# Performance work log

Measured on AMD Instinct MI355X. Metric: run time of the kernel, lower is better.

The kernel has to match this reference:

```python
import jax, jax.numpy as jnp
import numpy as np

N_LAYERS = 4
BATCH, IN_DIM, N_UNITS, OUT_DIM = 65536, 16, 1024, 1


def _linear(x, w, b):
    return x @ w.T + b


def setup_inputs() -> dict:
    key = jax.random.key(0)
    ks = jax.random.split(key, 18)
    s = lambda fan_in: 1.0 / np.sqrt(fan_in)
    return {
        "x": jax.random.normal(ks[0], (BATCH, IN_DIM), jnp.float32),
        "Sw_w": jax.random.normal(ks[1], (N_UNITS, IN_DIM), jnp.float32) * s(IN_DIM),
        "Sw_b": jax.random.normal(ks[2], (N_UNITS,), jnp.float32) * 0.01,
        "Uz_w": jax.random.normal(ks[3], (N_UNITS, IN_DIM), jnp.float32) * s(IN_DIM),
        "Uz_b": jax.random.normal(ks[4], (N_UNITS,), jnp.float32) * 0.01,
        "Wz_w": jax.random.normal(ks[5], (N_UNITS, N_UNITS), jnp.float32) * s(N_UNITS),
        "Wz_b": jax.random.normal(ks[6], (N_UNITS,), jnp.float32) * 0.01,
        "Ug_w": jax.random.normal(ks[7], (N_UNITS, IN_DIM), jnp.float32) * s(IN_DIM),
        "Ug_b": jax.random.normal(ks[8], (N_UNITS,), jnp.float32) * 0.01,
        "Wg_w": jax.random.normal(ks[9], (N_UNITS, N_UNITS), jnp.float32) * s(N_UNITS),
        "Wg_b": jax.random.normal(ks[10], (N_UNITS,), jnp.float32) * 0.01,
        "Ur_w": jax.random.normal(ks[11], (N_UNITS, IN_DIM), jnp.float32) * s(IN_DIM),
        "Ur_b": jax.random.normal(ks[12], (N_UNITS,), jnp.float32) * 0.01,
        "Uh_w": jax.random.normal(ks[13], (N_UNITS, IN_DIM), jnp.float32) * s(IN_DIM),
        "Uh_b": jax.random.normal(ks[14], (N_UNITS,), jnp.float32) * 0.01,
        "out_w": jax.random.normal(ks[15], (OUT_DIM, N_UNITS), jnp.float32) * s(N_UNITS),
        "out_b": jax.random.normal(ks[16], (OUT_DIM,), jnp.float32) * 0.01,
    }


def reference(x, Sw_w, Sw_b, Uz_w, Uz_b, Wz_w, Wz_b, Ug_w, Ug_b, Wg_w, Wg_b,
              Ur_w, Ur_b, Uh_w, Uh_b, out_w, out_b):
    act = jnp.tanh
    S1 = _linear(x, Sw_w, Sw_b)  # [B, H]
    # x-side projections are loop-invariant; hoist them.
    ux_z = _linear(x, Uz_w, Uz_b)
    ux_g = _linear(x, Ug_w, Ug_b)
    ux_r = _linear(x, Ur_w, Ur_b)
    ux_h = _linear(x, Uh_w, Uh_b)
    # NOTE: original forward uses Wg (not Wr/Wh) in the R and H gates — replicated faithfully.
    wgS1 = _linear(S1, Wg_w, Wg_b)  # G depends only on S1: loop-invariant
    output = None
    for i in range(N_LAYERS):
        S = S1 if i == 0 else act(output)
        Z = act(ux_z + _linear(S, Wz_w, Wz_b))
        G = act(ux_g + wgS1)
        R = act(ux_r + _linear(S, Wg_w, Wg_b))
        H = act(ux_h + _linear(S * R, Wg_w, Wg_b))
        output = (1.0 - G) * H + Z * S
    return _linear(output, out_w, out_b)
```

## Files before the change

kernel.cpp:

```cpp
#include <hip/hip_runtime.h>
#include <hip/hip_bf16.h>


typedef float f32x4 __attribute__((ext_vector_type(4)));
typedef __bf16 bf16x8 __attribute__((ext_vector_type(8)));
typedef unsigned int u32x4 __attribute__((ext_vector_type(4)));

#define MFMA16 __builtin_amdgcn_mfma_f32_16x16x32_bf16

#define WS_WZ   0u
#define WS_WG   (2u << 20)
#define WS_XT   (4u << 20)
#define WS_BIAS ((4u << 20) + 6u * 65536u)
#define WS_GB   ((size_t)8 << 20)
#define WS_ZB   (WS_GB + ((size_t)32 << 20))
#define WS_NEED2 (WS_ZB + ((size_t)32 << 20))

static __device__ __forceinline__ unsigned short f2bf(float f) {
    __hip_bfloat16 h = __float2bfloat16(f);
    union { __hip_bfloat16 h; unsigned short u; } c; c.h = h; return c.u;
}
static __device__ __forceinline__ float bf2f(unsigned short u) {
    union { unsigned int u; float f; } c; c.u = ((unsigned int)u) << 16; return c.f;
}
static __device__ __forceinline__ float fast_tanh(float x) {
    float e = __expf(2.0f * x);
    return 1.0f - 2.0f * __builtin_amdgcn_rcpf(e + 1.0f);
}
static __device__ __forceinline__ unsigned int swoff(int row, int kelem) {
    unsigned int a = (unsigned int)(row * 2048 + kelem * 2);
    return a ^ (unsigned int)((row & 7) << 4);
}
static __device__ __forceinline__ u32x4 ntl4(const void* p) {
    return __builtin_nontemporal_load((const u32x4*)p);
}
static __device__ __forceinline__ void nts4(void* p, u32x4 v) {
    __builtin_nontemporal_store(v, (u32x4*)p);
}

__global__ void prep_big(const float* __restrict__ Wz, const float* __restrict__ Wg,
                         char* __restrict__ ws) {
    int bid = blockIdx.x;
    int mat = bid >> 11, rem = bid & 2047;
    int ks = rem >> 6, cf = rem & 63;
    const float* src = mat ? Wg : Wz;
    char* dst = ws + ((size_t)mat << 21) + ((size_t)(ks * 64 + cf) << 10);
    int l = threadIdx.x;
    int col = cf * 16 + (l & 15);
    int kb  = ks * 32 + ((l >> 4) << 3);
    unsigned short* d = (unsigned short*)(dst + l * 16);
    #pragma unroll
    for (int j = 0; j < 8; ++j) d[j] = f2bf(src[col * 1024 + kb + j]);
}

__global__ void prep_x(const float* __restrict__ Uz, const float* __restrict__ Ur,
                       const float* __restrict__ Uh, const float* __restrict__ Ug,
                       const float* __restrict__ Sw, char* __restrict__ xt) {
    int bid = blockIdx.x;
    int g_ = bid >> 6, cf = bid & 63;
    int l = threadIdx.x;
    int col = cf * 16 + (l & 15);
    int kb  = (l >> 4) << 3;
    unsigned short* d = (unsigned short*)(xt + ((size_t)(g_ * 64 + cf) << 10) + l * 16);
    #pragma unroll
    for (int j = 0; j < 8; ++j) {
        int k = kb + j;
        float v = 0.0f;
        if (k < 16) {
            int idx = col * 16 + k;
            switch (g_) {
                case 0: v = Uz[idx]; break;
                case 1: v = Ur[idx]; break;
                case 2: v = Uh[idx]; break;
                case 3: v = Ug[idx]; break;
                case 4: v = Ur[idx] - Ug[idx]; break;
                case 5: v = Sw[idx]; break;
            }
        }
        d[j] = f2bf(v);
    }
}

__global__ void prep_bias(const float* __restrict__ Uz_b, const float* __restrict__ Wz_b,
                          const float* __restrict__ Ur_b, const float* __restrict__ Uh_b,
                          const float* __restrict__ Ug_b, const float* __restrict__ Wg_b,
                          const float* __restrict__ Sw_b, float* __restrict__ dst) {
    int i = blockIdx.x * 256 + threadIdx.x;
    dst[i]        = Uz_b[i] + Wz_b[i];
    dst[1024 + i] = Ur_b[i] + Wg_b[i];
    dst[2048 + i] = Uh_b[i] + Wg_b[i];
    dst[3072 + i] = Ug_b[i] + Wg_b[i];
    dst[4096 + i] = Sw_b[i];
}

static __device__ __forceinline__ void stage_xb(const float* __restrict__ x,
                                                unsigned short* xb, int t, int tid) {
    for (int i = tid; i < 64 * 32; i += 1024) {
        int r = i >> 5, c = i & 31;
        float v = (c < 16) ? x[(size_t)(t * 64 + r) * 16 + c] : 0.0f;
        xb[i] = f2bf(v);
    }
}

static __device__ __forceinline__ void mmx16(f32x4 (&acc)[4][4], const char* __restrict__ xtab,
                                             const unsigned short* xb, int lane, int wv) {
    const int c15 = lane & 15, h = lane >> 4;
    bf16x8 a[4];
    #pragma unroll
    for (int rf = 0; rf < 4; ++rf)
        a[rf] = *(const bf16x8*)(xb + (c15 + 16 * rf) * 32 + h * 8);
    #pragma unroll
    for (int cf = 0; cf < 4; ++cf) {
        bf16x8 b = *(const bf16x8*)(xtab + ((wv * 4 + cf) << 10) + lane * 16);
        #pragma unroll
        for (int rf = 0; rf < 4; ++rf) acc[rf][cf] = MFMA16(a[rf], b, acc[rf][cf], 0, 0, 0);
    }
}

static __device__ __forceinline__ void mms16(f32x4 (&acc)[4][4], const char* __restrict__ stab,
                                             const char* sb, int lane, int wv) {
    const int c15 = lane & 15, h = lane >> 4;
    #pragma unroll 2
    for (int ks = 0; ks < 32; ++ks) {
        const char* bp = stab + ((size_t)(ks * 64 + wv * 4) << 10) + lane * 16;
        bf16x8 b[4];
        #pragma unroll
        for (int cf = 0; cf < 4; ++cf) b[cf] = *(const bf16x8*)(bp + (cf << 10));
        bf16x8 a[4];
        #pragma unroll
        for (int rf = 0; rf < 4; ++rf)
            a[rf] = *(const bf16x8*)(sb + swoff(c15 + 16 * rf, (ks << 5) + (h << 3)));
        #pragma unroll
        for (int cf = 0; cf < 4; ++cf)
            #pragma unroll
            for (int rf = 0; rf < 4; ++rf)
                acc[rf][cf] = MFMA16(a[rf], b[cf], acc[rf][cf], 0, 0, 0);
    }
}

#define ZERO_ACC(acc) { _Pragma("unroll") for (int rf_ = 0; rf_ < 4; ++rf_) \
    _Pragma("unroll") for (int cf_ = 0; cf_ < 4; ++cf_) acc[rf_][cf_] = (f32x4)0.0f; }

__global__ __launch_bounds__(1024, 4)
void mega(const float* __restrict__ x, const char* __restrict__ ws,
          const float* __restrict__ ow, const float* __restrict__ ob,
          float* __restrict__ outp, char* __restrict__ Gb, char* __restrict__ Zb) {
    extern __shared__ char lds[];
    char* sbuf = lds;
    unsigned short* xb = (unsigned short*)(lds + 131072);
    float* red = (float*)(lds + 131072 + 4096);
    const int tid = threadIdx.x, lane = tid & 63, wv = tid >> 6;
    const int c15 = lane & 15, h = lane >> 4;
    const int wg = blockIdx.x;
    char* gslot = Gb + ((size_t)wg << 17);
    char* zslot = Zb + ((size_t)wg << 17);

    const float* BZ = (const float*)(ws + WS_BIAS);
    const float* BR = BZ + 1024;
    const float* BH = BZ + 2048;
    const float* BG = BZ + 3072;
    const float* BS = BZ + 4096;

    #pragma clang loop unroll(disable)
    for (int rt = 0; rt < 4; ++rt) {
        const int t = rt * 256 + wg;
        stage_xb(x, xb, t, tid);
        __syncthreads();

        f32x4 acc[4][4];
        ZERO_ACC(acc);
        mmx16(acc, ws + WS_XT + 5 * 65536, xb, lane, wv);
        #pragma unroll
        for (int cf = 0; cf < 4; ++cf) {
            int col = (wv << 6) + (cf << 4) + c15;
            float b = BS[col];
            #pragma unroll
            for (int rf = 0; rf < 4; ++rf)
                #pragma unroll
                for (int r = 0; r < 4; ++r) {
                    int row = (rf << 4) + (h << 2) + r;
                    *(unsigned short*)(sbuf + swoff(row, col)) = f2bf(acc[rf][cf][r] + b);
                }
        }
        __syncthreads();

        ZERO_ACC(acc);
        mmx16(acc, ws + WS_XT + 3 * 65536, xb, lane, wv);
        mms16(acc, ws + WS_WG, sbuf, lane, wv);
        {
            unsigned int pk[32];
            #pragma unroll
            for (int cf = 0; cf < 4; ++cf) {
                int col = (wv << 6) + (cf << 4) + c15;
                float b = BG[col];
                #pragma unroll
                for (int rf = 0; rf < 4; ++rf) {
                    float v[4];
                    #pragma unroll
                    for (int r = 0; r < 4; ++r) v[r] = fast_tanh(acc[rf][cf][r] + b);
                    pk[(rf * 4 + cf) * 2 + 0] = (unsigned int)f2bf(v[0]) | ((unsigned int)f2bf(v[1]) << 16);
                    pk[(rf * 4 + cf) * 2 + 1] = (unsigned int)f2bf(v[2]) | ((unsigned int)f2bf(v[3]) << 16);
                }
            }
            #pragma unroll
            for (int w = 0; w < 8; ++w) {
                u32x4 q = { pk[w * 4], pk[w * 4 + 1], pk[w * 4 + 2], pk[w * 4 + 3] };
                nts4(gslot + w * 16384 + tid * 16, q);
            }
        }

        #pragma clang loop unroll(disable)
        for (int L = 0; L < 4; ++L) {
            ZERO_ACC(acc);
            mmx16(acc, ws + WS_XT + 0 * 65536, xb, lane, wv);
            mms16(acc, ws + WS_WZ, sbuf, lane, wv);
            {
                unsigned int pk[32];
                #pragma unroll
                for (int cf = 0; cf < 4; ++cf) {
                    int col = (wv << 6) + (cf << 4) + c15;
                    float bzl = BZ[col];
                    #pragma unroll
                    for (int rf = 0; rf < 4; ++rf) {
                        float v[4];
                        #pragma unroll
                        for (int r = 0; r < 4; ++r) {
                            int row = (rf << 4) + (h << 2) + r;
                            float z = fast_tanh(acc[rf][cf][r] + bzl);
                            v[r] = z * bf2f(*(const unsigned short*)(sbuf + swoff(row, col)));
                        }
                        pk[(rf * 4 + cf) * 2 + 0] = (unsigned int)f2bf(v[0]) | ((unsigned int)f2bf(v[1]) << 16);
                        pk[(rf * 4 + cf) * 2 + 1] = (unsigned int)f2bf(v[2]) | ((unsigned int)f2bf(v[3]) << 16);
                    }
                }
                #pragma unroll
                for (int w = 0; w < 8; ++w) {
                    u32x4 q = { pk[w * 4], pk[w * 4 + 1], pk[w * 4 + 2], pk[w * 4 + 3] };
                    nts4(zslot + w * 16384 + tid * 16, q);
                }
            }

            ZERO_ACC(acc);
            mmx16(acc, ws + WS_XT + 1 * 65536, xb, lane, wv);
            mms16(acc, ws + WS_WG, sbuf, lane, wv);
            {
                unsigned int srp[32];
                #pragma unroll
                for (int cf = 0; cf < 4; ++cf) {
                    int col = (wv << 6) + (cf << 4) + c15;
                    float brl = BR[col];
                    #pragma unroll
                    for (int rf = 0; rf < 4; ++rf) {
                        float v[4];
                        #pragma unroll
                        for (int r = 0; r < 4; ++r) {
                            int row = (rf << 4) + (h << 2) + r;
                            float rv = fast_tanh(acc[rf][cf][r] + brl);
                            v[r] = rv * bf2f(*(const unsigned short*)(sbuf + swoff(row, col)));
                        }
                        srp[(rf * 4 + cf) * 2 + 0] = (unsigned int)f2bf(v[0]) | ((unsigned int)f2bf(v[1]) << 16);
                        srp[(rf * 4 + cf) * 2 + 1] = (unsigned int)f2bf(v[2]) | ((unsigned int)f2bf(v[3]) << 16);
                    }
                }
                __syncthreads();
                #pragma unroll
                for (int cf = 0; cf < 4; ++cf) {
                    int col = (wv << 6) + (cf << 4) + c15;
                    #pragma unroll
                    for (int rf = 0; rf < 4; ++rf)
                        #pragma unroll
                        for (int r = 0; r < 4; ++r) {
                            int row = (rf << 4) + (h << 2) + r;
                            unsigned short u = (unsigned short)((srp[(rf * 4 + cf) * 2 + (r >> 1)] >> ((r & 1) * 16)) & 0xffff);
                            *(unsigned short*)(sbuf + swoff(row, col)) = u;
                        }
                }
            }
            __syncthreads();

            ZERO_ACC(acc);
            mmx16(acc, ws + WS_XT + 2 * 65536, xb, lane, wv);
            mms16(acc, ws + WS_WG, sbuf, lane, wv);
            __syncthreads();

            if (L < 3) {
                #pragma unroll
                for (int w = 0; w < 8; ++w) {
                    u32x4 g4 = ntl4(gslot + w * 16384 + tid * 16);
                    u32x4 z4 = ntl4(zslot + w * 16384 + tid * 16);
                    #pragma unroll
                    for (int jj = 0; jj < 2; ++jj) {
                        int rfcf = w * 2 + jj;
                        int rf = rfcf >> 2, cf = rfcf & 3;
                        int col = (wv << 6) + (cf << 4) + c15;
                        float bhl = BH[col];
                        #pragma unroll
                        for (int r = 0; r < 4; ++r) {
                            int row = (rf << 4) + (h << 2) + r;
                            float g  = bf2f((unsigned short)((g4[jj * 2 + (r >> 1)] >> ((r & 1) * 16)) & 0xffff));
                            float zs = bf2f((unsigned short)((z4[jj * 2 + (r >> 1)] >> ((r & 1) * 16)) & 0xffff));
                            float hv = fast_tanh(acc[rf][cf][r] + bhl);
                            float o  = (1.0f - g) * hv + zs;
                            *(unsigned short*)(sbuf + swoff(row, col)) = f2bf(fast_tanh(o));
                        }
                    }
                }
                __syncthreads();
            } else {
                float po[16];
                #pragma unroll
                for (int i = 0; i < 16; ++i) po[i] = 0.0f;
                #pragma unroll
                for (int w = 0; w < 8; ++w) {
                    u32x4 g4 = ntl4(gslot + w * 16384 + tid * 16);
                    u32x4 z4 = ntl4(zslot + w * 16384 + tid * 16);
                    #pragma unroll
                    for (int jj = 0; jj < 2; ++jj) {
                        int rfcf = w * 2 + jj;
                        int rf = rfcf >> 2, cf = rfcf & 3;
                        int col = (wv << 6) + (cf << 4) + c15;
                        float bhl = BH[col];
                        float oww = ow[col];
                        #pragma unroll
                        for (int r = 0; r < 4; ++r) {
                            float g  = bf2f((unsigned short)((g4[jj * 2 + (r >> 1)] >> ((r & 1) * 16)) & 0xffff));
                            float zs = bf2f((unsigned short)((z4[jj * 2 + (r >> 1)] >> ((r & 1) * 16)) & 0xffff));
                            float hv = fast_tanh(acc[rf][cf][r] + bhl);
                            po[(rf << 2) + r] += ((1.0f - g) * hv + zs) * oww;
                        }
                    }
                }
                #pragma unroll
                for (int off = 1; off < 16; off <<= 1)
                    #pragma unroll
                    for (int i = 0; i < 16; ++i) po[i] += __shfl_xor(po[i], off);
                if (c15 == 0) {
                    #pragma unroll
                    for (int rf = 0; rf < 4; ++rf)
                        #pragma unroll
                        for (int r = 0; r < 4; ++r)
                            red[wv * 64 + (rf << 4) + (h << 2) + r] = po[(rf << 2) + r];
                }
                __syncthreads();
                if (tid < 64) {
                    float s = ob[0];
                    #pragma unroll
                    for (int w = 0; w < 16; ++w) s += red[w * 64 + tid];
                    outp[t * 64 + tid] = s;
                }
                __syncthreads();
            }
        }
    }
}


static __device__ __forceinline__ void mm_x(f32x4 acc[2][8], const char* __restrict__ xtab,
                                            const unsigned short* __restrict__ xb,
                                            int lane, int wv) {
    const int c15 = lane & 15, h = lane >> 4;
    bf16x8 a0 = *(const bf16x8*)(xb + c15 * 48 + h * 8);
    bf16x8 a1 = *(const bf16x8*)(xb + (c15 + 16) * 48 + h * 8);
    #pragma unroll
    for (int cf = 0; cf < 8; ++cf) {
        bf16x8 b = *(const bf16x8*)(xtab + ((wv * 8 + cf) << 10) + lane * 16);
        acc[0][cf] = MFMA16(a0, b, acc[0][cf], 0, 0, 0);
        acc[1][cf] = MFMA16(a1, b, acc[1][cf], 0, 0, 0);
    }
}

static __device__ __forceinline__ void mm_s(f32x4 acc[2][8], const char* __restrict__ stab,
                                            const char* __restrict__ sb, int lane, int wv) {
    const int c15 = lane & 15, h = lane >> 4;
    #pragma unroll 2
    for (int ks = 0; ks < 32; ++ks) {
        const char* bp = stab + ((size_t)(ks * 64 + wv * 8) << 10) + lane * 16;
        bf16x8 b[8];
        #pragma unroll
        for (int cf = 0; cf < 8; ++cf) b[cf] = *(const bf16x8*)(bp + (cf << 10));
        bf16x8 a0 = *(const bf16x8*)(sb + swoff(c15,      (ks << 5) + (h << 3)));
        bf16x8 a1 = *(const bf16x8*)(sb + swoff(c15 + 16, (ks << 5) + (h << 3)));
        #pragma unroll
        for (int cf = 0; cf < 8; ++cf) {
            acc[0][cf] = MFMA16(a0, b[cf], acc[0][cf], 0, 0, 0);
            acc[1][cf] = MFMA16(a1, b[cf], acc[1][cf], 0, 0, 0);
        }
    }
}

__global__ __launch_bounds__(512, 2)
void dgm_main(const float* __restrict__ x, const float* __restrict__ out_w,
              const float* __restrict__ out_b, const char* __restrict__ ws,
              float* __restrict__ out) {
    extern __shared__ char lds[];
    char* sbuf0 = lds;
    char* sbuf1 = lds + 65536;
    unsigned short* xb = (unsigned short*)(lds + 131072);
    float* red = (float*)(lds + 131072 + 3072);

    const int tid = threadIdx.x, lane = tid & 63, wv = tid >> 6;
    const int c15 = lane & 15, h = lane >> 4;
    const int t = blockIdx.x;

    const char* WZ = ws + WS_WZ;
    const char* WG = ws + WS_WG;
    const char* XT = ws + WS_XT;
    const float* BZ = (const float*)(ws + WS_BIAS);
    const float* BR = BZ + 1024;
    const float* BH = BZ + 2048;
    const float* BG = BZ + 3072;
    const float* BS = BZ + 4096;

    for (int i = tid; i < 32 * 48; i += 512) {
        int r_ = i / 48, c_ = i % 48;
        float v = (c_ < 16) ? x[(t * 32 + r_) * 16 + c_] : 0.0f;
        xb[r_ * 48 + c_] = f2bf(v);
    }
    __syncthreads();

    f32x4 acc[2][8];
    unsigned int g1m[2][8][2];
    unsigned int zs[2][8][2];
    float po[8];
    #pragma unroll
    for (int i = 0; i < 8; ++i) po[i] = 0.0f;

    #pragma unroll
    for (int rf = 0; rf < 2; ++rf)
        #pragma unroll
        for (int cf = 0; cf < 8; ++cf) acc[rf][cf] = (f32x4)0.0f;
    mm_x(acc, XT + 5 * 65536, xb, lane, wv);
    #pragma unroll
    for (int cf = 0; cf < 8; ++cf) {
        int col = (wv << 7) + (cf << 4) + c15;
        float b = BS[col];
        #pragma unroll
        for (int rf = 0; rf < 2; ++rf)
            #pragma unroll
            for (int r = 0; r < 4; ++r) {
                int row = (rf << 4) + (h << 2) + r;
                *(unsigned short*)(sbuf0 + swoff(row, col)) = f2bf(acc[rf][cf][r] + b);
            }
    }
    __syncthreads();

    {
        #pragma unroll
        for (int rf = 0; rf < 2; ++rf)
            #pragma unroll
            for (int cf = 0; cf < 8; ++cf) acc[rf][cf] = (f32x4)0.0f;
        mm_x(acc, XT + 3 * 65536, xb, lane, wv);
        mm_s(acc, WG, sbuf0, lane, wv);
        unsigned int wgx[2][8][2];
        #pragma unroll
        for (int rf = 0; rf < 2; ++rf)
            #pragma unroll
            for (int cf = 0; cf < 8; ++cf) {
                wgx[rf][cf][0] = (unsigned int)f2bf(acc[rf][cf][0]) |
                                 ((unsigned int)f2bf(acc[rf][cf][1]) << 16);
                wgx[rf][cf][1] = (unsigned int)f2bf(acc[rf][cf][2]) |
                                 ((unsigned int)f2bf(acc[rf][cf][3]) << 16);
            }
        #pragma unroll
        for (int rf = 0; rf < 2; ++rf)
            #pragma unroll
            for (int cf = 0; cf < 8; ++cf) acc[rf][cf] = (f32x4)0.0f;
        mm_x(acc, XT + 4 * 65536, xb, lane, wv);
        #pragma unroll
        for (int cf = 0; cf < 8; ++cf) {
            int col = (wv << 7) + (cf << 4) + c15;
            float brl = BR[col], bgl = BG[col];
            #pragma unroll
            for (int rf = 0; rf < 2; ++rf) {
                float g1v[4];
                #pragma unroll
                for (int r = 0; r < 4; ++r) {
                    int row = (rf << 4) + (h << 2) + r;
                    float wgv = bf2f((unsigned short)((wgx[rf][cf][r >> 1] >> ((r & 1) * 16)) & 0xffff));
                    float rv = fast_tanh(wgv + acc[rf][cf][r] + brl);
                    float s1 = bf2f(*(const unsigned short*)(sbuf0 + swoff(row, col)));
                    *(unsigned short*)(sbuf1 + swoff(row, col)) = f2bf(s1 * rv);
                    g1v[r] = 1.0f - fast_tanh(wgv + bgl);
                }
                g1m[rf][cf][0] = (unsigned int)f2bf(g1v[0]) | ((unsigned int)f2bf(g1v[1]) << 16);
                g1m[rf][cf][1] = (unsigned int)f2bf(g1v[2]) | ((unsigned int)f2bf(g1v[3]) << 16);
            }
        }
    }
    __syncthreads();

    char* cur = sbuf0;
    char* oth = sbuf1;
    #pragma clang loop unroll(disable)
    for (int L = 0; L < 4; ++L) {
        #pragma unroll
        for (int rf = 0; rf < 2; ++rf)
            #pragma unroll
            for (int cf = 0; cf < 8; ++cf) acc[rf][cf] = (f32x4)0.0f;
        mm_x(acc, XT + 0 * 65536, xb, lane, wv);
        mm_s(acc, WZ, cur, lane, wv);
        #pragma unroll
        for (int cf = 0; cf < 8; ++cf) {
            int col = (wv << 7) + (cf << 4) + c15;
            float bzl = BZ[col];
            #pragma unroll
            for (int rf = 0; rf < 2; ++rf) {
                float zv[4];
                #pragma unroll
                for (int r = 0; r < 4; ++r) {
                    int row = (rf << 4) + (h << 2) + r;
                    float z = fast_tanh(acc[rf][cf][r] + bzl);
                    float s = bf2f(*(const unsigned short*)(cur + swoff(row, col)));
                    zv[r] = z * s;
                }
                zs[rf][cf][0] = (unsigned int)f2bf(zv[0]) | ((unsigned int)f2bf(zv[1]) << 16);
                zs[rf][cf][1] = (unsigned int)f2bf(zv[2]) | ((unsigned int)f2bf(zv[3]) << 16);
            }
        }
        if (L > 0) {
            #pragma unroll
            for (int rf = 0; rf < 2; ++rf)
                #pragma unroll
                for (int cf = 0; cf < 8; ++cf) acc[rf][cf] = (f32x4)0.0f;
            mm_x(acc, XT + 1 * 65536, xb, lane, wv);
            mm_s(acc, WG, cur, lane, wv);
            #pragma unroll
            for (int cf = 0; cf < 8; ++cf) {
                int col = (wv << 7) + (cf << 4) + c15;
                float brl = BR[col];
                #pragma unroll
                for (int rf = 0; rf < 2; ++rf)
                    #pragma unroll
                    for (int r = 0; r < 4; ++r) {
                        int row = (rf << 4) + (h << 2) + r;
                        float rv = fast_tanh(acc[rf][cf][r] + brl);
                        float s = bf2f(*(const unsigned short*)(cur + swoff(row, col)));
                        *(unsigned short*)(oth + swoff(row, col)) = f2bf(s * rv);
                    }
            }
        }
        __syncthreads();
        #pragma unroll
        for (int rf = 0; rf < 2; ++rf)
            #pragma unroll
            for (int cf = 0; cf < 8; ++cf) acc[rf][cf] = (f32x4)0.0f;
        mm_x(acc, XT + 2 * 65536, xb, lane, wv);
        mm_s(acc, WG, oth, lane, wv);
        __syncthreads();
        if (L < 3) {
            #pragma unroll
            for (int cf = 0; cf < 8; ++cf) {
                int col = (wv << 7) + (cf << 4) + c15;
                float bhl = BH[col];
                #pragma unroll
                for (int rf = 0; rf < 2; ++rf)
                    #pragma unroll
                    for (int r = 0; r < 4; ++r) {
                        int row = (rf << 4) + (h << 2) + r;
                        float hv = fast_tanh(acc[rf][cf][r] + bhl);
                        float g1 = bf2f((unsigned short)((g1m[rf][cf][r >> 1] >> ((r & 1) * 16)) & 0xffff));
                        float zsv = bf2f((unsigned short)((zs[rf][cf][r >> 1] >> ((r & 1) * 16)) & 0xffff));
                        float o = g1 * hv + zsv;
                        *(unsigned short*)(oth + swoff(row, col)) = f2bf(fast_tanh(o));
                    }
            }
        } else {
            #pragma unroll
            for (int cf = 0; cf < 8; ++cf) {
                int col = (wv << 7) + (cf << 4) + c15;
                float bhl = BH[col];
                float oww = out_w[col];
                #pragma unroll
                for (int rf = 0; rf < 2; ++rf)
                    #pragma unroll
                    for (int r = 0; r < 4; ++r) {
                        float hv = fast_tanh(acc[rf][cf][r] + bhl);
                        float g1 = bf2f((unsigned short)((g1m[rf][cf][r >> 1] >> ((r & 1) * 16)) & 0xffff));
                        float zsv = bf2f((unsigned short)((zs[rf][cf][r >> 1] >> ((r & 1) * 16)) & 0xffff));
                        po[(rf << 2) + r] += (g1 * hv + zsv) * oww;
                    }
            }
        }
        __syncthreads();
        char* tmp = cur; cur = oth; oth = tmp;
    }

    #pragma unroll
    for (int off = 1; off < 16; off <<= 1)
        #pragma unroll
        for (int i = 0; i < 8; ++i) po[i] += __shfl_xor(po[i], off);
    if (c15 == 0) {
        #pragma unroll
        for (int rf = 0; rf < 2; ++rf)
            #pragma unroll
            for (int r = 0; r < 4; ++r)
                red[wv * 32 + (rf << 4) + (h << 2) + r] = po[(rf << 2) + r];
    }
    __syncthreads();
    if (tid < 32) {
        float s = out_b[0];
        #pragma unroll
        for (int w = 0; w < 8; ++w) s += red[w * 32 + tid];
        out[t * 32 + tid] = s;
    }
}

extern "C" void kernel_launch(void* const* d_in, const int* in_sizes, int n_in,
                              void* d_out, int out_size, void* d_ws, size_t ws_size,
                              hipStream_t stream) {
    (void)in_sizes; (void)n_in; (void)out_size;
    const float* x    = (const float*)d_in[0];
    const float* Sw_w = (const float*)d_in[1];
    const float* Sw_b = (const float*)d_in[2];
    const float* Uz_w = (const float*)d_in[3];
    const float* Uz_b = (const float*)d_in[4];
    const float* Wz_w = (const float*)d_in[5];
    const float* Wz_b = (const float*)d_in[6];
    const float* Ug_w = (const float*)d_in[7];
    const float* Ug_b = (const float*)d_in[8];
    const float* Wg_w = (const float*)d_in[9];
    const float* Wg_b = (const float*)d_in[10];
    const float* Ur_w = (const float*)d_in[11];
    const float* Ur_b = (const float*)d_in[12];
    const float* Uh_w = (const float*)d_in[13];
    const float* Uh_b = (const float*)d_in[14];
    const float* ow   = (const float*)d_in[15];
    const float* ob   = (const float*)d_in[16];
    char* ws = (char*)d_ws;

    prep_big<<<4096, 64, 0, stream>>>(Wz_w, Wg_w, ws);
    prep_x<<<384, 64, 0, stream>>>(Uz_w, Ur_w, Uh_w, Ug_w, Sw_w, ws + WS_XT);
    prep_bias<<<4, 256, 0, stream>>>(Uz_b, Wz_b, Ur_b, Uh_b, Ug_b, Wg_b, Sw_b,
                                     (float*)(ws + WS_BIAS));

    if (ws_size >= WS_NEED2) {
        const int LM = 131072 + 4096 + 4096;
        hipFuncSetAttribute(reinterpret_cast<const void*>(mega),
                            hipFuncAttributeMaxDynamicSharedMemorySize, LM);
        mega<<<256, 1024, LM, stream>>>(x, ws, ow, ob, (float*)d_out,
                                        ws + WS_GB, ws + WS_ZB);
    } else {
        const int ldsBytes = 131072 + 3072 + 1024;
        hipFuncSetAttribute(reinterpret_cast<const void*>(dgm_main),
                            hipFuncAttributeMaxDynamicSharedMemorySize, ldsBytes);
        dgm_main<<<65536 / 32, 512, ldsBytes, stream>>>(x, ow, ob, ws, (float*)d_out);
    }
}
```

Before: 3.539 ms.

## Add soft grid barrier to keep workgroups in lockstep across weight passes

```diff
diff --git a/kernel.cpp b/kernel.cpp
--- a/kernel.cpp
+++ b/kernel.cpp
@@ -12,6 +12,7 @@
 #define WS_WG   (2u << 20)
 #define WS_XT   (4u << 20)
 #define WS_BIAS ((4u << 20) + 6u * 65536u)
+#define WS_CTR  (WS_BIAS + 24576u)
 #define WS_GB   ((size_t)8 << 20)
 #define WS_ZB   (WS_GB + ((size_t)32 << 20))
 #define WS_NEED2 (WS_ZB + ((size_t)32 << 20))
@@ -36,6 +37,23 @@
 }
 static __device__ __forceinline__ void nts4(void* p, u32x4 v) {
     __builtin_nontemporal_store(v, (u32x4*)p);
+}
+
+static __device__ __forceinline__ void soft_bar(unsigned int* ctr,
+                                                unsigned int target, int tid) {
+    __syncthreads();
+    if (tid == 0) {
+        atomicAdd(ctr, 1u);
+        int polls = 0;
+        while (polls < 400) {
+            unsigned int v = __hip_atomic_load(ctr, __ATOMIC_RELAXED,
+                                               __HIP_MEMORY_SCOPE_AGENT);
+            if (v >= target) break;
+            __builtin_amdgcn_s_sleep(2);
+            ++polls;
+        }
+    }
+    __syncthreads();
 }
 
 __global__ void prep_big(const float* __restrict__ Wz, const float* __restrict__ Wg,
@@ -84,13 +102,15 @@
 __global__ void prep_bias(const float* __restrict__ Uz_b, const float* __restrict__ Wz_b,
                           const float* __restrict__ Ur_b, const float* __restrict__ Uh_b,
                           const float* __restrict__ Ug_b, const float* __restrict__ Wg_b,
-                          const float* __restrict__ Sw_b, float* __restrict__ dst) {
+                          const float* __restrict__ Sw_b, float* __restrict__ dst,
+                          unsigned int* ctr) {
     int i = blockIdx.x * 256 + threadIdx.x;
     dst[i]        = Uz_b[i] + Wz_b[i];
     dst[1024 + i] = Ur_b[i] + Wg_b[i];
     dst[2048 + i] = Uh_b[i] + Wg_b[i];
     dst[3072 + i] = Ug_b[i] + Wg_b[i];
     dst[4096 + i] = Sw_b[i];
+    if (i == 0) *ctr = 0u;
 }
 
 static __device__ __forceinline__ void stage_xb(const float* __restrict__ x,
@@ -144,7 +164,8 @@
 __global__ __launch_bounds__(1024, 4)
 void mega(const float* __restrict__ x, const char* __restrict__ ws,
           const float* __restrict__ ow, const float* __restrict__ ob,
-          float* __restrict__ outp, char* __restrict__ Gb, char* __restrict__ Zb) {
+          float* __restrict__ outp, char* __restrict__ Gb, char* __restrict__ Zb,
+          unsigned int* ctr) {
     extern __shared__ char lds[];
     char* sbuf = lds;
     unsigned short* xb = (unsigned short*)(lds + 131072);
@@ -161,6 +182,8 @@
     const float* BG = BZ + 3072;
     const float* BS = BZ + 4096;
 
+    unsigned int bidx = 0;
+
     #pragma clang loop unroll(disable)
     for (int rt = 0; rt < 4; ++rt) {
         const int t = rt * 256 + wg;
@@ -184,6 +207,7 @@
         }
         __syncthreads();
 
+        soft_bar(ctr, 256u * (++bidx), tid);
         ZERO_ACC(acc);
         mmx16(acc, ws + WS_XT + 3 * 65536, xb, lane, wv);
         mms16(acc, ws + WS_WG, sbuf, lane, wv);
@@ -211,6 +235,7 @@
 
         #pragma clang loop unroll(disable)
         for (int L = 0; L < 4; ++L) {
+            soft_bar(ctr, 256u * (++bidx), tid);
             ZERO_ACC(acc);
             mmx16(acc, ws + WS_XT + 0 * 65536, xb, lane, wv);
             mms16(acc, ws + WS_WZ, sbuf, lane, wv);
@@ -240,6 +265,7 @@
                 }
             }
 
+            soft_bar(ctr, 256u * (++bidx), tid);
             ZERO_ACC(acc);
             mmx16(acc, ws + WS_XT + 1 * 65536, xb, lane, wv);
             mms16(acc, ws + WS_WG, sbuf, lane, wv);
@@ -627,18 +653,19 @@
     const float* ow   = (const float*)d_in[15];
     const float* ob   = (const float*)d_in[16];
     char* ws = (char*)d_ws;
+    unsigned int* ctr = (unsigned int*)(ws + WS_CTR);
 
     prep_big<<<4096, 64, 0, stream>>>(Wz_w, Wg_w, ws);
     prep_x<<<384, 64, 0, stream>>>(Uz_w, Ur_w, Uh_w, Ug_w, Sw_w, ws + WS_XT);
     prep_bias<<<4, 256, 0, stream>>>(Uz_b, Wz_b, Ur_b, Uh_b, Ug_b, Wg_b, Sw_b,
-                                     (float*)(ws + WS_BIAS));
+                                     (float*)(ws + WS_BIAS), ctr);
 
     if (ws_size >= WS_NEED2) {
         const int LM = 131072 + 4096 + 4096;
         hipFuncSetAttribute(reinterpret_cast<const void*>(mega),
                             hipFuncAttributeMaxDynamicSharedMemorySize, LM);
         mega<<<256, 1024, LM, stream>>>(x, ws, ow, ob, (float*)d_out,
-                                        ws + WS_GB, ws + WS_ZB);
+                                        ws + WS_GB, ws + WS_ZB, ctr);
     } else {
         const int ldsBytes = 131072 + 3072 + 1024;
         hipFuncSetAttribute(reinterpret_cast<const void*>(dgm_main),
```

Measured after the change: 4.329 ms. +22.3%, slower.
